# Optimization experiments

Measured on AMD Instinct MI355X. Metric: run time of the kernel, lower is better.

Reference implementation:

```python
import jax, jax.numpy as jnp
import numpy as np

D_MODEL = 1024
N_HEADS = 16
D_K = D_MODEL // N_HEADS


def setup_inputs() -> dict:
    key = jax.random.key(0)
    ks = jax.random.split(key, 9)
    s = 0.02
    x = jax.random.normal(ks[0], (2, 2048, D_MODEL), dtype=jnp.float32)
    Wq = jax.random.normal(ks[1], (D_MODEL, D_MODEL), dtype=jnp.float32) * s
    bq = jax.random.normal(ks[2], (D_MODEL,), dtype=jnp.float32) * s
    Wk = jax.random.normal(ks[3], (D_MODEL, D_MODEL), dtype=jnp.float32) * s
    bk = jax.random.normal(ks[4], (D_MODEL,), dtype=jnp.float32) * s
    Wv = jax.random.normal(ks[5], (D_MODEL, D_MODEL), dtype=jnp.float32) * s
    bv = jax.random.normal(ks[6], (D_MODEL,), dtype=jnp.float32) * s
    Wo = jax.random.normal(ks[7], (D_MODEL, D_MODEL), dtype=jnp.float32) * s
    bo = jax.random.normal(ks[8], (D_MODEL,), dtype=jnp.float32) * s
    return {"x": x, "Wq": Wq, "bq": bq, "Wk": Wk, "bk": bk,
            "Wv": Wv, "bv": bv, "Wo": Wo, "bo": bo}


def reference(x, Wq, bq, Wk, bk, Wv, bv, Wo, bo):
    B, S, D = x.shape
    # nn.Linear: y = x @ W.T + b
    q = x @ Wq.T + bq  # [B,S,D]
    k = x @ Wk.T + bk
    v = x @ Wv.T + bv
    # split heads -> [B,H,S,dk]
    q = q.reshape(B, S, N_HEADS, D_K).transpose(0, 2, 1, 3)
    k = k.reshape(B, S, N_HEADS, D_K).transpose(0, 2, 1, 3)
    v = v.reshape(B, S, N_HEADS, D_K).transpose(0, 2, 1, 3)
    scale = 1.0 / jnp.sqrt(jnp.asarray(D_K, dtype=x.dtype))
    scores = jnp.einsum('bhqd,bhkd->bhqk', q, k) * scale  # [B,H,S,S]
    weights = jax.nn.softmax(scores, axis=-1)
    out = jnp.einsum('bhqk,bhkd->bhqd', weights, v)  # [B,H,S,dk]
    concat = out.transpose(0, 2, 1, 3).reshape(B, S, D)
    return concat @ Wo.T + bo
```

## Files before the change

kernel.cpp:

```cpp
#include <hip/hip_runtime.h>

typedef unsigned short ushort_t;
typedef __attribute__((ext_vector_type(8))) __bf16 bf16x8;
typedef __attribute__((ext_vector_type(4))) float floatx4;

#define AS1 __attribute__((address_space(1)))
#define AS3 __attribute__((address_space(3)))

#define D_MODEL 1024
#define NH 16
#define DKH 64
#define SEQ 2048
#define NB 2
#define MTOT (NB * SEQ)

#define QSCALE 0.18033688011112042f

#define OFF_X   0u
#define OFF_WQ  4194304u
#define OFF_BQ  5242880u
#define OFF_WK  5243904u
#define OFF_BK  6292480u
#define OFF_WV  6293504u
#define OFF_BV  7342080u
#define OFF_WO  7343104u
#define OFF_BO  8391680u
#define CVT_TOT 8392704u

__device__ __forceinline__ float bf2f(ushort_t u) {
    union { unsigned u; float f; } v; v.u = ((unsigned)u) << 16; return v.f;
}
__device__ __forceinline__ ushort_t f2bf(float f) {
    union { float f; unsigned u; } v; v.f = f;
    unsigned r = v.u + 0x7FFFu + ((v.u >> 16) & 1u);
    return (ushort_t)(r >> 16);
}
__device__ __forceinline__ unsigned pack2bf(float a, float b) {
    unsigned ua = __float_as_uint(a), ub = __float_as_uint(b);
    ua = ua + 0x7FFFu + ((ua >> 16) & 1u);
    ub = ub + 0x7FFFu + ((ub >> 16) & 1u);
    return __builtin_amdgcn_perm(ub, ua, 0x07060302);
}

__global__ __launch_bounds__(256) void convert_kernel(
    const float* __restrict__ x,  const float* __restrict__ wq, const float* __restrict__ bq_,
    const float* __restrict__ wk, const float* __restrict__ bk_, const float* __restrict__ wv,
    const float* __restrict__ bv_, const float* __restrict__ wo, const float* __restrict__ bo_,
    ushort_t* __restrict__ dst)
{
    const unsigned idx = ((unsigned)blockIdx.x * 256u + threadIdx.x) * 4u;
    if (idx >= CVT_TOT) return;
    const float* src; unsigned off;
    if      (idx < OFF_WQ) { src = x;   off = idx; }
    else if (idx < OFF_BQ) { src = wq;  off = idx - OFF_WQ; }
    else if (idx < OFF_WK) { src = bq_; off = idx - OFF_BQ; }
    else if (idx < OFF_BK) { src = wk;  off = idx - OFF_WK; }
    else if (idx < OFF_WV) { src = bk_; off = idx - OFF_BK; }
    else if (idx < OFF_BV) { src = wv;  off = idx - OFF_WV; }
    else if (idx < OFF_WO) { src = bv_; off = idx - OFF_BV; }
    else if (idx < OFF_BO) { src = wo;  off = idx - OFF_WO; }
    else                   { src = bo_; off = idx - OFF_BO; }
    float4 v = *reinterpret_cast<const float4*>(src + off);
    uint2 p;
    p.x = pack2bf(v.x, v.y);
    p.y = pack2bf(v.z, v.w);
    *reinterpret_cast<uint2*>(dst + idx) = p;
}

__device__ __forceinline__ void gemm_core(
    const ushort_t* __restrict__ X, const ushort_t* __restrict__ W,
    int m0, int n0, ushort_t* As, ushort_t* Bs, floatx4 acc[4][4])
{
    const int tid = threadIdx.x;
    const int lane = tid & 63, wv = tid >> 6;
    const int wm = (wv >> 1) * 64, wn = (wv & 1) * 64;
    const int l15 = lane & 15, quad = lane >> 4;
    const floatx4 z4 = {0.f, 0.f, 0.f, 0.f};
#pragma unroll
    for (int i = 0; i < 4; ++i)
#pragma unroll
        for (int j = 0; j < 4; ++j) acc[i][j] = z4;
    const int lrow = lane >> 2;
    const int lcol = (lane & 3) * 8;
    const ushort_t* gA = X + (size_t)(m0 + lrow) * D_MODEL + lcol;
    const ushort_t* gB = W + (size_t)(n0 + lrow) * D_MODEL + lcol;
    for (int k0 = 0; k0 < D_MODEL; k0 += 32) {
        __syncthreads();
#pragma unroll
        for (int j = 0; j < 2; ++j) {
            const int r0 = (wv * 2 + j) * 16;
            __builtin_amdgcn_global_load_lds(
                (const AS1 unsigned*)(gA + (size_t)r0 * D_MODEL + k0),
                (AS3 unsigned*)(As + r0 * 32), 16, 0, 0);
            __builtin_amdgcn_global_load_lds(
                (const AS1 unsigned*)(gB + (size_t)r0 * D_MODEL + k0),
                (AS3 unsigned*)(Bs + r0 * 32), 16, 0, 0);
        }
        asm volatile("s_waitcnt vmcnt(0)" ::: "memory");
        __syncthreads();
        bf16x8 af[4], bfr[4];
#pragma unroll
        for (int i = 0; i < 4; ++i)
            af[i] = *reinterpret_cast<const bf16x8*>(As + (wm + i * 16 + l15) * 32 + quad * 8);
#pragma unroll
        for (int j = 0; j < 4; ++j)
            bfr[j] = *reinterpret_cast<const bf16x8*>(Bs + (wn + j * 16 + l15) * 32 + quad * 8);
#pragma unroll
        for (int i = 0; i < 4; ++i)
#pragma unroll
            for (int j = 0; j < 4; ++j)
                acc[i][j] = __builtin_amdgcn_mfma_f32_16x16x32_bf16(af[i], bfr[j], acc[i][j], 0, 0, 0);
    }
}

__global__ __launch_bounds__(256, 3) void qkv_kernel(
    const ushort_t* __restrict__ x,
    const ushort_t* __restrict__ Wq, const ushort_t* __restrict__ bq,
    const ushort_t* __restrict__ Wk, const ushort_t* __restrict__ bk,
    const ushort_t* __restrict__ Wv, const ushort_t* __restrict__ bv,
    ushort_t* __restrict__ q_ws, ushort_t* __restrict__ k_ws, ushort_t* __restrict__ vt_ws)
{
    __shared__ __align__(16) ushort_t lds[17408];
    ushort_t* As = lds;
    ushort_t* Bs = lds + 128 * 32;
    const int m0 = blockIdx.x * 128;
    const int which = blockIdx.y >> 3;
    const int n0 = (blockIdx.y & 7) * 128;
    const ushort_t* W    = (which == 0) ? Wq : (which == 1) ? Wk : Wv;
    const ushort_t* bias = (which == 0) ? bq : (which == 1) ? bk : bv;
    floatx4 acc[4][4];
    gemm_core(x, W, m0, n0, As, Bs, acc);
    const int tid = threadIdx.x, lane = tid & 63, wv = tid >> 6;
    const int wm = (wv >> 1) * 64, wn = (wv & 1) * 64;
    const int l15 = lane & 15, quad = lane >> 4;
    const int b0 = m0 >> 11;
    if (which < 2) {
        ushort_t* dst = (which == 0) ? q_ws : k_ws;
        const float scl = (which == 0) ? QSCALE : 1.0f;
#pragma unroll
        for (int j = 0; j < 4; ++j) {
            int n = n0 + wn + j * 16 + l15;
            float bb = bf2f(bias[n]);
            int h = n >> 6, d = n & 63;
#pragma unroll
            for (int i = 0; i < 4; ++i)
#pragma unroll
                for (int r = 0; r < 4; ++r) {
                    int m = m0 + wm + i * 16 + quad * 4 + r;
                    int s = m & (SEQ - 1);
                    dst[(((size_t)(b0 * NH + h)) * SEQ + s) * DKH + d] = f2bf((acc[i][j][r] + bb) * scl);
                }
        }
    } else {
        __syncthreads();
        ushort_t* Ts = lds;
#pragma unroll
        for (int j = 0; j < 4; ++j) {
            int coln = wn + j * 16 + l15;
            float bb = bf2f(bias[n0 + coln]);
#pragma unroll
            for (int i = 0; i < 4; ++i)
#pragma unroll
                for (int r = 0; r < 4; ++r) {
                    int rowm = wm + i * 16 + quad * 4 + r;
                    Ts[coln * 136 + rowm] = f2bf(acc[i][j][r] + bb);
                }
        }
        __syncthreads();
        const int s0 = m0 & (SEQ - 1);
#pragma unroll
        for (int i = 0; i < 8; ++i) {
            int c = tid + 256 * i;
            int nr = c >> 4, mc = (c & 15) * 8;
            float4 v = *reinterpret_cast<const float4*>(Ts + nr * 136 + mc);
            int n = n0 + nr, h = n >> 6, d = n & 63;
            *reinterpret_cast<float4*>(vt_ws + (((size_t)(b0 * NH + h)) * DKH + d) * SEQ + s0 + mc) = v;
        }
    }
}

__global__ __launch_bounds__(256, 4) void attn_kernel(
    const ushort_t* __restrict__ q_ws, const ushort_t* __restrict__ k_ws,
    const ushort_t* __restrict__ vt_ws, ushort_t* __restrict__ concat)
{
    __shared__ __align__(16) ushort_t sm[3 * 64 * 72];
    ushort_t* Ks  = sm;
    ushort_t* VTs = sm + 4608;
    ushort_t* Ps  = sm + 9216;

    const int qb = blockIdx.x;
    const int bh = blockIdx.y;
    const int tid = threadIdx.x;
    const int lane = tid & 63, wv = tid >> 6;
    const int l15 = lane & 15, quad = lane >> 4;

    const ushort_t* Qg = q_ws + ((size_t)bh * SEQ + qb * 64) * DKH;
    const ushort_t* Kg = k_ws + (size_t)bh * SEQ * DKH;
    const ushort_t* Vg = vt_ws + (size_t)bh * DKH * SEQ;

#pragma unroll
    for (int i = 0; i < 2; ++i) {
        int c = tid + 256 * i;
        int row = c >> 3, col = (c & 7) * 8;
        *reinterpret_cast<float4*>(Ps + row * 72 + col) =
            *reinterpret_cast<const float4*>(Qg + row * DKH + col);
    }
    __syncthreads();
    bf16x8 aq[2];
#pragma unroll
    for (int ks = 0; ks < 2; ++ks)
        aq[ks] = *reinterpret_cast<const bf16x8*>(Ps + (wv * 16 + l15) * 72 + ks * 32 + quad * 8);

    const floatx4 z4 = {0.f, 0.f, 0.f, 0.f};
    floatx4 o[4];
#pragma unroll
    for (int dt = 0; dt < 4; ++dt) o[dt] = z4;
    float lacc = 0.f;

    for (int kt = 0; kt < SEQ; kt += 64) {
        __syncthreads();
#pragma unroll
        for (int i = 0; i < 2; ++i) {
            int c = tid + 256 * i;
            int row = c >> 3, col = (c & 7) * 8;
            *reinterpret_cast<float4*>(Ks + row * 72 + col) =
                *reinterpret_cast<const float4*>(Kg + (size_t)(kt + row) * DKH + col);
            *reinterpret_cast<float4*>(VTs + row * 72 + col) =
                *reinterpret_cast<const float4*>(Vg + (size_t)row * SEQ + kt + col);
        }
        __syncthreads();

        floatx4 st[4];
#pragma unroll
        for (int mt = 0; mt < 4; ++mt) st[mt] = z4;
#pragma unroll
        for (int ks = 0; ks < 2; ++ks)
#pragma unroll
            for (int mt = 0; mt < 4; ++mt) {
                bf16x8 akf = *reinterpret_cast<const bf16x8*>(Ks + (mt * 16 + l15) * 72 + ks * 32 + quad * 8);
                st[mt] = __builtin_amdgcn_mfma_f32_16x16x32_bf16(akf, aq[ks], st[mt], 0, 0, 0);
            }

#pragma unroll
        for (int mt = 0; mt < 4; ++mt)
#pragma unroll
            for (int r = 0; r < 4; ++r) {
                float p = exp2f(st[mt][r]);
                st[mt][r] = p;
                lacc += p;
            }
#pragma unroll
        for (int mt = 0; mt < 4; ++mt) {
            uint2 pk;
            pk.x = pack2bf(st[mt][0], st[mt][1]);
            pk.y = pack2bf(st[mt][2], st[mt][3]);
            *reinterpret_cast<uint2*>(Ps + (wv * 16 + l15) * 72 + mt * 16 + quad * 4) = pk;
        }
        asm volatile("s_waitcnt lgkmcnt(0)" ::: "memory");
#pragma unroll
        for (int ks = 0; ks < 2; ++ks) {
            bf16x8 ap = *reinterpret_cast<const bf16x8*>(Ps + (wv * 16 + l15) * 72 + ks * 32 + quad * 8);
#pragma unroll
            for (int dt = 0; dt < 4; ++dt) {
                bf16x8 bvv = *reinterpret_cast<const bf16x8*>(VTs + (dt * 16 + l15) * 72 + ks * 32 + quad * 8);
                o[dt] = __builtin_amdgcn_mfma_f32_16x16x32_bf16(ap, bvv, o[dt], 0, 0, 0);
            }
        }
    }
    lacc += __shfl_xor(lacc, 16, 64);
    lacc += __shfl_xor(lacc, 32, 64);
    float linv = 1.f / lacc;

    const int b0 = bh >> 4, h = bh & 15;
    const int s0 = qb * 64 + wv * 16;
#pragma unroll
    for (int r = 0; r < 4; ++r) {
        float lB = __shfl(linv, quad * 4 + r, 64);
        int row = s0 + quad * 4 + r;
        size_t base = ((size_t)(b0 * SEQ + row)) * D_MODEL + h * DKH;
#pragma unroll
        for (int dt = 0; dt < 4; ++dt)
            concat[base + dt * 16 + l15] = f2bf(o[dt][r] * lB);
    }
}

__global__ __launch_bounds__(256, 3) void oproj_kernel(
    const ushort_t* __restrict__ cc, const ushort_t* __restrict__ Wo,
    const ushort_t* __restrict__ bo, float* __restrict__ out)
{
    __shared__ __align__(16) ushort_t lds[2 * 128 * 32];
    ushort_t* As = lds;
    ushort_t* Bs = lds + 128 * 32;
    const int m0 = blockIdx.x * 128, n0 = blockIdx.y * 128;
    floatx4 acc[4][4];
    gemm_core(cc, Wo, m0, n0, As, Bs, acc);
    const int tid = threadIdx.x, lane = tid & 63, wv = tid >> 6;
    const int wm = (wv >> 1) * 64, wn = (wv & 1) * 64;
    const int l15 = lane & 15, quad = lane >> 4;
#pragma unroll
    for (int j = 0; j < 4; ++j) {
        int n = n0 + wn + j * 16 + l15;
        float bb = bf2f(bo[n]);
#pragma unroll
        for (int i = 0; i < 4; ++i)
#pragma unroll
            for (int r = 0; r < 4; ++r) {
                int m = m0 + wm + i * 16 + quad * 4 + r;
                out[(size_t)m * D_MODEL + n] = acc[i][j][r] + bb;
            }
    }
}

extern "C" void kernel_launch(void* const* d_in, const int* in_sizes, int n_in,
                              void* d_out, int out_size, void* d_ws, size_t ws_size,
                              hipStream_t stream)
{
    ushort_t* cvt = (ushort_t*)d_ws;
    const ushort_t* xb  = cvt + OFF_X;
    const ushort_t* Wqb = cvt + OFF_WQ;
    const ushort_t* bqb = cvt + OFF_BQ;
    const ushort_t* Wkb = cvt + OFF_WK;
    const ushort_t* bkb = cvt + OFF_BK;
    const ushort_t* Wvb = cvt + OFF_WV;
    const ushort_t* bvb = cvt + OFF_BV;
    const ushort_t* Wob = cvt + OFF_WO;
    const ushort_t* bob = cvt + OFF_BO;
    ushort_t* q_ws   = cvt + CVT_TOT;
    ushort_t* k_ws   = q_ws  + (size_t)MTOT * D_MODEL;
    ushort_t* vt_ws  = k_ws  + (size_t)MTOT * D_MODEL;
    ushort_t* concat = vt_ws + (size_t)MTOT * D_MODEL;

    convert_kernel<<<(CVT_TOT / 1024), 256, 0, stream>>>(
        (const float*)d_in[0], (const float*)d_in[1], (const float*)d_in[2],
        (const float*)d_in[3], (const float*)d_in[4], (const float*)d_in[5],
        (const float*)d_in[6], (const float*)d_in[7], (const float*)d_in[8], cvt);
    qkv_kernel<<<dim3(32, 24), 256, 0, stream>>>(xb, Wqb, bqb, Wkb, bkb, Wvb, bvb, q_ws, k_ws, vt_ws);
    attn_kernel<<<dim3(32, 32), 256, 0, stream>>>(q_ws, k_ws, vt_ws, concat);
    oproj_kernel<<<dim3(32, 8), 256, 0, stream>>>(concat, Wob, bob, (float*)d_out);
}
```

Before: 213.0 us.

## Split attention keys across two wave groups and stage Q/K writes via LDS

The attention kernel now uses 512 threads per block handling 128 query rows. Two halves of the block each process half of the key sequence and are merged through LDS at the end, and each wave handles 32 query rows so every loaded K fragment feeds two MFMAs. Separately, the Q/K projection epilogue is staged through LDS so that global stores are 16-byte vectorized instead of scattered 2-byte stores. The cost is more LDS per block, an extra reduction and sync at the end, and half as many blocks in the grid.

Measured after the change: 210.2 us. About the same (-1.3%).

```diff
diff --git a/kernel.cpp b/kernel.cpp
--- a/kernel.cpp
+++ b/kernel.cpp
@@ -134,25 +134,35 @@
     const int wm = (wv >> 1) * 64, wn = (wv & 1) * 64;
     const int l15 = lane & 15, quad = lane >> 4;
     const int b0 = m0 >> 11;
+    const int s0 = m0 & (SEQ - 1);
+    __syncthreads();
     if (which < 2) {
+        ushort_t* Ts = lds;
         ushort_t* dst = (which == 0) ? q_ws : k_ws;
         const float scl = (which == 0) ? QSCALE : 1.0f;
 #pragma unroll
         for (int j = 0; j < 4; ++j) {
-            int n = n0 + wn + j * 16 + l15;
-            float bb = bf2f(bias[n]);
-            int h = n >> 6, d = n & 63;
+            int coln = wn + j * 16 + l15;
+            float bb = bf2f(bias[n0 + coln]);
 #pragma unroll
             for (int i = 0; i < 4; ++i)
 #pragma unroll
                 for (int r = 0; r < 4; ++r) {
-                    int m = m0 + wm + i * 16 + quad * 4 + r;
-                    int s = m & (SEQ - 1);
-                    dst[(((size_t)(b0 * NH + h)) * SEQ + s) * DKH + d] = f2bf((acc[i][j][r] + bb) * scl);
+                    int rowm = wm + i * 16 + quad * 4 + r;
+                    Ts[rowm * 136 + coln] = f2bf((acc[i][j][r] + bb) * scl);
                 }
         }
+        __syncthreads();
+#pragma unroll
+        for (int i = 0; i < 8; ++i) {
+            int c = tid + 256 * i;
+            int rowm = c >> 4, chunk = c & 15;
+            float4 v = *reinterpret_cast<const float4*>(Ts + rowm * 136 + chunk * 8);
+            int s = s0 + rowm;
+            int n = n0 + chunk * 8, h = n >> 6, d = n & 63;
+            *reinterpret_cast<float4*>(dst + (((size_t)(b0 * NH + h)) * SEQ + s) * DKH + d) = v;
+        }
     } else {
-        __syncthreads();
         ushort_t* Ts = lds;
 #pragma unroll
         for (int j = 0; j < 4; ++j) {
@@ -167,7 +177,6 @@
                 }
         }
         __syncthreads();
-        const int s0 = m0 & (SEQ - 1);
 #pragma unroll
         for (int i = 0; i < 8; ++i) {
             int c = tid + 256 * i;
@@ -179,108 +188,149 @@
     }
 }
 
-__global__ __launch_bounds__(256, 4) void attn_kernel(
+__global__ __launch_bounds__(512, 4) void attn_kernel(
     const ushort_t* __restrict__ q_ws, const ushort_t* __restrict__ k_ws,
     const ushort_t* __restrict__ vt_ws, ushort_t* __restrict__ concat)
 {
-    __shared__ __align__(16) ushort_t sm[3 * 64 * 72];
-    ushort_t* Ks  = sm;
-    ushort_t* VTs = sm + 4608;
-    ushort_t* Ps  = sm + 9216;
-
-    const int qb = blockIdx.x;
-    const int bh = blockIdx.y;
+    __shared__ __align__(16) ushort_t sm[36864];
+    const int qb = blockIdx.x, bh = blockIdx.y;
     const int tid = threadIdx.x;
     const int lane = tid & 63, wv = tid >> 6;
+    const int half = wv >> 2, wq = wv & 3;
     const int l15 = lane & 15, quad = lane >> 4;
-
-    const ushort_t* Qg = q_ws + ((size_t)bh * SEQ + qb * 64) * DKH;
-    const ushort_t* Kg = k_ws + (size_t)bh * SEQ * DKH;
-    const ushort_t* Vg = vt_ws + (size_t)bh * DKH * SEQ;
+    const int ht = tid & 255;
+
+    const ushort_t* Qg = q_ws + ((size_t)bh * SEQ + qb * 128) * DKH;
+    const ushort_t* Kg = k_ws + ((size_t)bh * SEQ + half * (SEQ / 2)) * DKH;
+    const ushort_t* Vg = vt_ws + (size_t)bh * DKH * SEQ + half * (SEQ / 2);
+
+    ushort_t* Ks     = sm + half * 4608;
+    ushort_t* VTs    = sm + 9216 + half * 4608;
+    ushort_t* Ps     = sm + 18432 + wv * 2304;
+    ushort_t* Qstage = sm + 18432;
 
 #pragma unroll
     for (int i = 0; i < 2; ++i) {
-        int c = tid + 256 * i;
+        int c = tid + 512 * i;
         int row = c >> 3, col = (c & 7) * 8;
-        *reinterpret_cast<float4*>(Ps + row * 72 + col) =
+        *reinterpret_cast<float4*>(Qstage + row * 72 + col) =
             *reinterpret_cast<const float4*>(Qg + row * DKH + col);
     }
     __syncthreads();
-    bf16x8 aq[2];
-#pragma unroll
-    for (int ks = 0; ks < 2; ++ks)
-        aq[ks] = *reinterpret_cast<const bf16x8*>(Ps + (wv * 16 + l15) * 72 + ks * 32 + quad * 8);
+    bf16x8 aq[2][2];
+#pragma unroll
+    for (int nt = 0; nt < 2; ++nt)
+#pragma unroll
+        for (int ks = 0; ks < 2; ++ks)
+            aq[nt][ks] = *reinterpret_cast<const bf16x8*>(Qstage + (wq * 32 + nt * 16 + l15) * 72 + ks * 32 + quad * 8);
 
     const floatx4 z4 = {0.f, 0.f, 0.f, 0.f};
-    floatx4 o[4];
-#pragma unroll
-    for (int dt = 0; dt < 4; ++dt) o[dt] = z4;
-    float lacc = 0.f;
-
-    for (int kt = 0; kt < SEQ; kt += 64) {
+    floatx4 o[2][4];
+    float lacc[2] = {0.f, 0.f};
+#pragma unroll
+    for (int nt = 0; nt < 2; ++nt)
+#pragma unroll
+        for (int dt = 0; dt < 4; ++dt) o[nt][dt] = z4;
+
+    for (int t = 0; t < 16; ++t) {
         __syncthreads();
 #pragma unroll
         for (int i = 0; i < 2; ++i) {
-            int c = tid + 256 * i;
+            int c = ht + 256 * i;
             int row = c >> 3, col = (c & 7) * 8;
             *reinterpret_cast<float4*>(Ks + row * 72 + col) =
-                *reinterpret_cast<const float4*>(Kg + (size_t)(kt + row) * DKH + col);
+                *reinterpret_cast<const float4*>(Kg + (size_t)(t * 64 + row) * DKH + col);
             *reinterpret_cast<float4*>(VTs + row * 72 + col) =
-                *reinterpret_cast<const float4*>(Vg + (size_t)row * SEQ + kt + col);
-        }
-        __syncthreads();
-
-        floatx4 st[4];
-#pragma unroll
-        for (int mt = 0; mt < 4; ++mt) st[mt] = z4;
+                *reinterpret_cast<const float4*>(Vg + (size_t)row * SEQ + t * 64 + col);
+        }
+        __syncthreads();
+
+        floatx4 st[2][4];
+#pragma unroll
+        for (int nt = 0; nt < 2; ++nt)
+#pragma unroll
+            for (int mt = 0; mt < 4; ++mt) st[nt][mt] = z4;
 #pragma unroll
         for (int ks = 0; ks < 2; ++ks)
 #pragma unroll
             for (int mt = 0; mt < 4; ++mt) {
                 bf16x8 akf = *reinterpret_cast<const bf16x8*>(Ks + (mt * 16 + l15) * 72 + ks * 32 + quad * 8);
-                st[mt] = __builtin_amdgcn_mfma_f32_16x16x32_bf16(akf, aq[ks], st[mt], 0, 0, 0);
-            }
-
-#pragma unroll
-        for (int mt = 0; mt < 4; ++mt)
-#pragma unroll
-            for (int r = 0; r < 4; ++r) {
-                float p = exp2f(st[mt][r]);
-                st[mt][r] = p;
-                lacc += p;
-            }
-#pragma unroll
-        for (int mt = 0; mt < 4; ++mt) {
-            uint2 pk;
-            pk.x = pack2bf(st[mt][0], st[mt][1]);
-            pk.y = pack2bf(st[mt][2], st[mt][3]);
-            *reinterpret_cast<uint2*>(Ps + (wv * 16 + l15) * 72 + mt * 16 + quad * 4) = pk;
-        }
+                st[0][mt] = __builtin_amdgcn_mfma_f32_16x16x32_bf16(akf, aq[0][ks], st[0][mt], 0, 0, 0);
+                st[1][mt] = __builtin_amdgcn_mfma_f32_16x16x32_bf16(akf, aq[1][ks], st[1][mt], 0, 0, 0);
+            }
+
+#pragma unroll
+        for (int nt = 0; nt < 2; ++nt)
+#pragma unroll
+            for (int mt = 0; mt < 4; ++mt)
+#pragma unroll
+                for (int r = 0; r < 4; ++r) {
+                    float p = exp2f(st[nt][mt][r]);
+                    st[nt][mt][r] = p;
+                    lacc[nt] += p;
+                }
+#pragma unroll
+        for (int nt = 0; nt < 2; ++nt)
+#pragma unroll
+            for (int mt = 0; mt < 4; ++mt) {
+                uint2 pk;
+                pk.x = pack2bf(st[nt][mt][0], st[nt][mt][1]);
+                pk.y = pack2bf(st[nt][mt][2], st[nt][mt][3]);
+                *reinterpret_cast<uint2*>(Ps + (nt * 16 + l15) * 72 + mt * 16 + quad * 4) = pk;
+            }
         asm volatile("s_waitcnt lgkmcnt(0)" ::: "memory");
 #pragma unroll
         for (int ks = 0; ks < 2; ++ks) {
-            bf16x8 ap = *reinterpret_cast<const bf16x8*>(Ps + (wv * 16 + l15) * 72 + ks * 32 + quad * 8);
+            bf16x8 ap0 = *reinterpret_cast<const bf16x8*>(Ps + l15 * 72 + ks * 32 + quad * 8);
+            bf16x8 ap1 = *reinterpret_cast<const bf16x8*>(Ps + (16 + l15) * 72 + ks * 32 + quad * 8);
 #pragma unroll
             for (int dt = 0; dt < 4; ++dt) {
                 bf16x8 bvv = *reinterpret_cast<const bf16x8*>(VTs + (dt * 16 + l15) * 72 + ks * 32 + quad * 8);
-                o[dt] = __builtin_amdgcn_mfma_f32_16x16x32_bf16(ap, bvv, o[dt], 0, 0, 0);
-            }
-        }
-    }
-    lacc += __shfl_xor(lacc, 16, 64);
-    lacc += __shfl_xor(lacc, 32, 64);
-    float linv = 1.f / lacc;
-
-    const int b0 = bh >> 4, h = bh & 15;
-    const int s0 = qb * 64 + wv * 16;
-#pragma unroll
-    for (int r = 0; r < 4; ++r) {
-        float lB = __shfl(linv, quad * 4 + r, 64);
-        int row = s0 + quad * 4 + r;
-        size_t base = ((size_t)(b0 * SEQ + row)) * D_MODEL + h * DKH;
-#pragma unroll
-        for (int dt = 0; dt < 4; ++dt)
-            concat[base + dt * 16 + l15] = f2bf(o[dt][r] * lB);
+                o[0][dt] = __builtin_amdgcn_mfma_f32_16x16x32_bf16(ap0, bvv, o[0][dt], 0, 0, 0);
+                o[1][dt] = __builtin_amdgcn_mfma_f32_16x16x32_bf16(ap1, bvv, o[1][dt], 0, 0, 0);
+            }
+        }
+    }
+#pragma unroll
+    for (int nt = 0; nt < 2; ++nt) {
+        lacc[nt] += __shfl_xor(lacc[nt], 16, 64);
+        lacc[nt] += __shfl_xor(lacc[nt], 32, 64);
+    }
+    __syncthreads();
+    float* Of = (float*)sm;
+    float* lf = Of + 128 * 68;
+    if (half == 1) {
+#pragma unroll
+        for (int nt = 0; nt < 2; ++nt) {
+            if (quad == 0) lf[wq * 32 + nt * 16 + l15] = lacc[nt];
+#pragma unroll
+            for (int r = 0; r < 4; ++r) {
+                int row = wq * 32 + nt * 16 + quad * 4 + r;
+#pragma unroll
+                for (int dt = 0; dt < 4; ++dt)
+                    Of[row * 68 + dt * 16 + l15] = o[nt][dt][r];
+            }
+        }
+    }
+    __syncthreads();
+    if (half == 0) {
+        const int b0 = bh >> 4, h = bh & 15;
+#pragma unroll
+        for (int nt = 0; nt < 2; ++nt) {
+            float ltot = lacc[nt] + lf[wq * 32 + nt * 16 + l15];
+            float linv = 1.f / ltot;
+#pragma unroll
+            for (int r = 0; r < 4; ++r) {
+                float lB = __shfl(linv, quad * 4 + r, 64);
+                int row = wq * 32 + nt * 16 + quad * 4 + r;
+                size_t base = ((size_t)(b0 * SEQ + qb * 128 + row)) * D_MODEL + h * DKH;
+#pragma unroll
+                for (int dt = 0; dt < 4; ++dt) {
+                    float sum = o[nt][dt][r] + Of[row * 68 + dt * 16 + l15];
+                    concat[base + dt * 16 + l15] = f2bf(sum * lB);
+                }
+            }
+        }
     }
 }
 
@@ -335,6 +385,6 @@
         (const float*)d_in[3], (const float*)d_in[4], (const float*)d_in[5],
         (const float*)d_in[6], (const float*)d_in[7], (const float*)d_in[8], cvt);
     qkv_kernel<<<dim3(32, 24), 256, 0, stream>>>(xb, Wqb, bqb, Wkb, bkb, Wvb, bvb, q_ws, k_ws, vt_ws);
-    attn_kernel<<<dim3(32, 32), 256, 0, stream>>>(q_ws, k_ws, vt_ws, concat);
+    attn_kernel<<<dim3(16, 32), 512, 0, stream>>>(q_ws, k_ws, vt_ws, concat);
     oproj_kernel<<<dim3(32, 8), 256, 0, stream>>>(concat, Wob, bob, (float*)d_out);
 }
```
